# Performance work log

Hardware: AMD Instinct MI355X
Metric: run time of the kernel (lower is better)

The kernel has to match this reference:

```python
import math
import jax, jax.numpy as jnp
import numpy as np

T_NHEAD = 4
S_NHEAD = 4


def _ln(x, s, b, eps=1e-5):
    m = jnp.mean(x, axis=-1, keepdims=True)
    v = jnp.mean((x - m) ** 2, axis=-1, keepdims=True)
    return (x - m) / jnp.sqrt(v + eps) * s + b


def _pos_encoding(T, D):
    pos = jnp.arange(T, dtype=jnp.float32)[:, None]
    div = jnp.exp(jnp.arange(0, D, 2, dtype=jnp.float32) * (-math.log(10000.0) / D))
    pe = jnp.zeros((T, D), dtype=jnp.float32)
    pe = pe.at[:, 0::2].set(jnp.sin(pos * div))
    pe = pe.at[:, 1::2].set(jnp.cos(pos * div))
    return pe


def _forward(industry_ids, stock_features, market_features, emb_table, gate_w, gate_b,
             proj_w, proj_b, t_qw, t_kw, t_vw, t_ow, t_ob, t_nx_s, t_nx_b, t_nf_s, t_nf_b,
             t_f1w, t_f1b, t_f2w, t_f2b, s_qw, s_kw, s_vw, s_ow, s_ob, s_nx_s, s_nx_b,
             s_ni_s, s_ni_b, s_nf_s, s_nf_b, s_f1w, s_f1b, s_f2w, s_f2b, ta_w, dec_w, dec_b):
    N, T, F = stock_features.shape
    D = proj_w.shape[1]
    # industry embedding lookup
    ind_emb = emb_table[industry_ids]  # [N, E]
    # market gate (last timestep only), beta=1.0, scaled by d_output=d_feat
    mkt = market_features[:, -1, :]
    gate = F * jax.nn.softmax(mkt @ gate_w + gate_b, axis=-1)  # [N, F]
    x = stock_features * gate[:, None, :]
    # feature projection + positional encoding
    x = x @ proj_w + proj_b  # [N, T, D]
    x = x + _pos_encoding(T, D)
    # ---- TAttention (per-stock temporal self-attention) ----
    hd = D // T_NHEAD
    xs = _ln(x, t_nx_s, t_nx_b)
    q = (xs @ t_qw).reshape(N, T, T_NHEAD, hd)
    k = (xs @ t_kw).reshape(N, T, T_NHEAD, hd)
    v = (xs @ t_vw).reshape(N, T, T_NHEAD, hd)
    scores = jnp.einsum('nthd,nshd->nhts', q, k) / math.sqrt(hd)
    attn = jax.nn.softmax(scores, axis=-1)
    o = jnp.einsum('nhts,nshd->nthd', attn, v).reshape(N, T, D)
    xt = x + (o @ t_ow + t_ob)
    y = _ln(xt, t_nf_s, t_nf_b)
    xt = xt + (jax.nn.relu(y @ t_f1w + t_f1b) @ t_f2w + t_f2b)
    # ---- TemporalAttention (aggregate over time) ----
    h = xt @ ta_w  # [N, T, D]
    lam = jax.nn.softmax(jnp.einsum('ntd,nd->nt', h, h[:, -1, :]), axis=1)
    z = jnp.einsum('nt,ntd->nd', lam, xt)  # [N, D]
    # ---- SAttention (cross-stock attention over N) ----
    shd = D // S_NHEAD
    zs = _ln(z, s_nx_s, s_nx_b)
    ins = _ln(ind_emb, s_ni_s, s_ni_b)
    qk_in = jnp.concatenate([zs, ins], axis=-1)  # [N, D+E]
    sq = (qk_in @ s_qw).reshape(N, S_NHEAD, shd)
    sk = (qk_in @ s_kw).reshape(N, S_NHEAD, shd)
    sv = (zs @ s_vw).reshape(N, S_NHEAD, shd)
    sc = jnp.einsum('nhd,mhd->hnm', sq, sk) / math.sqrt(shd)
    sa = jax.nn.softmax(sc, axis=-1)
    so = jnp.einsum('hnm,mhd->nhd', sa, sv).reshape(N, D)
    zt = z + (so @ s_ow + s_ob)
    yn = _ln(zt, s_nf_s, s_nf_b)
    zt = zt + (jax.nn.relu(yn @ s_f1w + s_f1b) @ s_f2w + s_f2b)
    # decoder
    return zt @ dec_w + dec_b  # [N, 1]


def setup_inputs() -> dict:
    key = jax.random.key(0)
    ks = iter(jax.random.split(key, 64))
    N, T, F, M, E, D = 4096, 64, 158, 64, 32, 256
    def rn(shape, s=0.05):
        return jax.random.normal(next(ks), shape, dtype=jnp.float32) * s
    return dict(
        industry_ids=jax.random.randint(next(ks), (N,), 0, 256, dtype=jnp.int32),
        stock_features=rn((N, T, F), 1.0),
        market_features=rn((N, T, M), 1.0),
        emb_table=rn((256, E)),
        gate_w=rn((M, F)), gate_b=jnp.zeros((F,), jnp.float32),
        proj_w=rn((F, D)), proj_b=jnp.zeros((D,), jnp.float32),
        t_qw=rn((D, D)), t_kw=rn((D, D)), t_vw=rn((D, D)),
        t_ow=rn((D, D)), t_ob=jnp.zeros((D,), jnp.float32),
        t_nx_s=jnp.ones((D,), jnp.float32), t_nx_b=jnp.zeros((D,), jnp.float32),
        t_nf_s=jnp.ones((D,), jnp.float32), t_nf_b=jnp.zeros((D,), jnp.float32),
        t_f1w=rn((D, D)), t_f1b=jnp.zeros((D,), jnp.float32),
        t_f2w=rn((D, D)), t_f2b=jnp.zeros((D,), jnp.float32),
        s_qw=rn((D + E, D)), s_kw=rn((D + E, D)), s_vw=rn((D, D)),
        s_ow=rn((D, D)), s_ob=jnp.zeros((D,), jnp.float32),
        s_nx_s=jnp.ones((D,), jnp.float32), s_nx_b=jnp.zeros((D,), jnp.float32),
        s_ni_s=jnp.ones((E,), jnp.float32), s_ni_b=jnp.zeros((E,), jnp.float32),
        s_nf_s=jnp.ones((D,), jnp.float32), s_nf_b=jnp.zeros((D,), jnp.float32),
        s_f1w=rn((D, D)), s_f1b=jnp.zeros((D,), jnp.float32),
        s_f2w=rn((D, D)), s_f2b=jnp.zeros((D,), jnp.float32),
        ta_w=rn((D, D)),
        dec_w=rn((D, 1)), dec_b=jnp.zeros((1,), jnp.float32),
    )


def reference(industry_ids, stock_features, market_features, emb_table, gate_w, gate_b,
              proj_w, proj_b, t_qw, t_kw, t_vw, t_ow, t_ob, t_nx_s, t_nx_b, t_nf_s, t_nf_b,
              t_f1w, t_f1b, t_f2w, t_f2b, s_qw, s_kw, s_vw, s_ow, s_ob, s_nx_s, s_nx_b,
              s_ni_s, s_ni_b, s_nf_s, s_nf_b, s_f1w, s_f1b, s_f2w, s_f2b, ta_w, dec_w, dec_b):
    return _forward(industry_ids, stock_features, market_features, emb_table, gate_w, gate_b,
                    proj_w, proj_b, t_qw, t_kw, t_vw, t_ow, t_ob, t_nx_s, t_nx_b, t_nf_s, t_nf_b,
                    t_f1w, t_f1b, t_f2w, t_f2b, s_qw, s_kw, s_vw, s_ow, s_ob, s_nx_s, s_nx_b,
                    s_ni_s, s_ni_b, s_nf_s, s_nf_b, s_f1w, s_f1b, s_f2w, s_f2b, ta_w, dec_w, dec_b)
```

## Files before the change

kernel.cpp:

```cpp
#include <hip/hip_runtime.h>

typedef _Float16 f16;
typedef _Float16 f16x8 __attribute__((ext_vector_type(8)));
typedef _Float16 f16x4 __attribute__((ext_vector_type(4)));
typedef float    f32x4 __attribute__((ext_vector_type(4)));

#define MFMA32(a,b,c) __builtin_amdgcn_mfma_f32_16x16x32_f16((a),(b),(c),0,0,0)
#define MFMA16(a,b,c) __builtin_amdgcn_mfma_f32_16x16x16f16((a),(b),(c),0,0,0)

__device__ __forceinline__ f32x4 zero4() { f32x4 v = {0.f,0.f,0.f,0.f}; return v; }
#define ZERO44(A) { _Pragma("unroll") for (int z1=0;z1<4;++z1){ _Pragma("unroll") for (int z2=0;z2<4;++z2) A[z1][z2] = zero4(); } }

constexpr size_t OFF_PROJ = 0;
constexpr size_t OFF_QW  = 40960;
constexpr size_t OFF_KW  = 106496;
constexpr size_t OFF_VW  = 172032;
constexpr size_t OFF_OW  = 237568;
constexpr size_t OFF_F1  = 303104;
constexpr size_t OFF_F2  = 368640;
constexpr size_t OFF_TA  = 434176;
constexpr size_t OFF_SQW = 499712;
constexpr size_t OFF_SKW = 573440;
constexpr size_t OFF_SVW = 647168;
constexpr size_t OFF_SOW = 712704;
constexpr size_t OFF_SF1 = 778240;
constexpr size_t OFF_SF2 = 843776;
constexpr size_t W_ELEMS = 909312;
constexpr size_t PE_B  = W_ELEMS*2;
constexpr size_t Z_B   = PE_B  + 64*256*4;
constexpr size_t QK_B  = Z_B   + 4096ull*256*4;
constexpr size_t SQ_B  = QK_B  + 4096ull*288*2;
constexpr size_t SK_B  = SQ_B  + 4096ull*256*2;
constexpr size_t SVT_B = SK_B  + 4096ull*256*2;
constexpr size_t SO_B  = SVT_B + 4096ull*256*2;

struct PrepArgs {
  const float* src[14];
  int K[14]; int Kp[14]; int off[14];
};

__global__ void prep_kernel(PrepArgs a, f16* __restrict__ wbuf, float* __restrict__ pe) {
  int wsel = blockIdx.y;
  int tid = threadIdx.x;
  if (wsel < 14) {
    const float* S = a.src[wsel];
    int K = a.K[wsel], Kp = a.Kp[wsel];
    f16* D = wbuf + a.off[wsel];
    int n = blockIdx.x*4 + (tid & 3);
    for (int k = (tid >> 2); k < Kp; k += 64) {
      float v = (k < K) ? S[(size_t)k*256 + n] : 0.f;
      D[(size_t)n*Kp + k] = (f16)v;
    }
  } else {
    int idx = blockIdx.x*256 + tid;
    int t = idx >> 8, d = idx & 255, i = d >> 1;
    float div = expf((float)(2*i) * (-9.210340371976184f/256.f));
    float ang = (float)t * div;
    pe[idx] = (d & 1) ? cosf(ang) : sinf(ang);
  }
}

__device__ __forceinline__ void ln64v(f16 (*src)[264], f16 (*dst)[264],
    const float* __restrict__ sc, const float* __restrict__ bi, int w, int lane) {
  int row = w*16 + (lane >> 2);
  int c0 = lane & 3;
  f16x8 v[8];
  float s = 0.f, s2 = 0.f;
  #pragma unroll
  for (int j = 0; j < 8; ++j) {
    v[j] = *(const f16x8*)&src[row][j*32 + c0*8];
    #pragma unroll
    for (int e = 0; e < 8; ++e) { float f = (float)v[j][e]; s += f; s2 += f*f; }
  }
  s  += __shfl_xor(s, 1);  s  += __shfl_xor(s, 2);
  s2 += __shfl_xor(s2, 1); s2 += __shfl_xor(s2, 2);
  float mean = s * (1.f/256.f);
  float rstd = rsqrtf(s2 * (1.f/256.f) - mean*mean + 1e-5f);
  #pragma unroll
  for (int j = 0; j < 8; ++j) {
    int c = j*32 + c0*8;
    f16x8 o;
    #pragma unroll
    for (int e = 0; e < 8; ++e)
      o[e] = (f16)(((float)v[j][e] - mean) * rstd * sc[c+e] + bi[c+e]);
    *(f16x8*)&dst[row][c] = o;
  }
}

template<int KSTEPS, int LDB>
__device__ __forceinline__ void gemm_ldsA(f16 (*A)[264], const f16* __restrict__ B,
                                          f32x4 (&acc)[4][4], int w, int l15, int g) {
  #pragma unroll 2
  for (int ks = 0; ks < KSTEPS; ++ks) {
    int kc = ks*32 + g*8;
    f16x8 av[4], bv[4];
    #pragma unroll
    for (int j = 0; j < 4; ++j) av[j] = *(const f16x8*)&A[j*16 + l15][kc];
    #pragma unroll
    for (int j = 0; j < 4; ++j) bv[j] = *(const f16x8*)(B + (size_t)(w*64 + j*16 + l15)*LDB + kc);
    #pragma unroll
    for (int mt = 0; mt < 4; ++mt) {
      #pragma unroll
      for (int nt = 0; nt < 4; ++nt)
        acc[mt][nt] = MFMA32(av[mt], bv[nt], acc[mt][nt]);
    }
  }
}

__device__ __forceinline__ void ffn_block(f16 (*res)[264], f16 (*y)[264], f16 (*u)[72],
    const f16* __restrict__ W1, const f16* __restrict__ W2,
    const float* __restrict__ b1, const float* __restrict__ b2,
    int w, int l15, int g) {
  f32x4 acc2[4][4]; ZERO44(acc2);
  for (int ch = 0; ch < 4; ++ch) {
    f32x4 ua[4];
    #pragma unroll
    for (int nt = 0; nt < 4; ++nt) ua[nt] = zero4();
    #pragma unroll 2
    for (int ks = 0; ks < 8; ++ks) {
      int kc = ks*32 + g*8;
      f16x8 av = *(const f16x8*)&y[w*16 + l15][kc];
      f16x8 bv[4];
      #pragma unroll
      for (int j = 0; j < 4; ++j) bv[j] = *(const f16x8*)(W1 + (size_t)(ch*64 + j*16 + l15)*256 + kc);
      #pragma unroll
      for (int nt = 0; nt < 4; ++nt) ua[nt] = MFMA32(av, bv[nt], ua[nt]);
    }
    __syncthreads();
    #pragma unroll
    for (int nt = 0; nt < 4; ++nt) {
      int col = nt*16 + l15;
      #pragma unroll
      for (int i = 0; i < 4; ++i) {
        float v = ua[nt][i] + b1[ch*64 + col];
        u[w*16 + g*4 + i][col] = (f16)fmaxf(v, 0.f);
      }
    }
    __syncthreads();
    #pragma unroll
    for (int ks = 0; ks < 2; ++ks) {
      int kc = ks*32 + g*8;
      f16x8 av[4], bv[4];
      #pragma unroll
      for (int j = 0; j < 4; ++j) av[j] = *(const f16x8*)&u[j*16 + l15][kc];
      #pragma unroll
      for (int j = 0; j < 4; ++j) bv[j] = *(const f16x8*)(W2 + (size_t)(w*64 + j*16 + l15)*256 + ch*64 + kc);
      #pragma unroll
      for (int mt = 0; mt < 4; ++mt) {
        #pragma unroll
        for (int nt = 0; nt < 4; ++nt)
          acc2[mt][nt] = MFMA32(av[mt], bv[nt], acc2[mt][nt]);
      }
    }
  }
  #pragma unroll
  for (int mt = 0; mt < 4; ++mt) {
    #pragma unroll
    for (int nt = 0; nt < 4; ++nt) {
      int col = w*64 + nt*16 + l15;
      #pragma unroll
      for (int i = 0; i < 4; ++i) {
        int row = mt*16 + g*4 + i;
        float v = (float)res[row][col] + acc2[mt][nt][i] + b2[col];
        res[row][col] = (f16)v;
      }
    }
  }
}

__global__ __launch_bounds__(256, 2) void temporal_kernel(
    const float* __restrict__ stock, const float* __restrict__ market,
    const float* __restrict__ gate_w, const float* __restrict__ gate_b,
    const float* __restrict__ proj_b, const float* __restrict__ t_ob,
    const float* __restrict__ t_nx_s, const float* __restrict__ t_nx_b,
    const float* __restrict__ t_nf_s, const float* __restrict__ t_nf_b,
    const float* __restrict__ t_f1b, const float* __restrict__ t_f2b,
    const f16* __restrict__ wbuf, const float* __restrict__ pe,
    float* __restrict__ zout)
{
  __shared__ __align__(16) f16 B[64][264];
  __shared__ __align__(16) f16 ub[64][40];
  __shared__ float gatev[160];
  __shared__ float mkt[64];
  __shared__ float red[66];

  const int tid = threadIdx.x;
  const int lane = tid & 63;
  const int w = tid >> 6;
  const int l15 = lane & 15;
  const int g = lane >> 4;
  const int n = blockIdx.x;

  f16x4 xres[4][4];

  if (tid < 64) mkt[tid] = market[(size_t)n*4096 + 63*64 + tid];
  __syncthreads();
  float logit = 0.f;
  if (tid < 158) {
    float acc = gate_b[tid];
    for (int m = 0; m < 64; ++m) acc += mkt[m] * gate_w[m*158 + tid];
    logit = acc;
  }
  if (tid < 160) gatev[tid] = (tid < 158) ? logit : -1e30f;
  __syncthreads();
  if (w == 0) {
    float v = fmaxf(gatev[lane], gatev[lane + 64]);
    if (lane < 32) v = fmaxf(v, gatev[lane + 128]);
    #pragma unroll
    for (int off = 32; off >= 1; off >>= 1) v = fmaxf(v, __shfl_xor(v, off));
    if (lane == 0) red[0] = v;
  }
  __syncthreads();
  float gmax = red[0];
  float ev = (tid < 158) ? __expf(logit - gmax) : 0.f;
  if (tid < 160) gatev[tid] = ev;
  __syncthreads();
  if (w == 0) {
    float v = gatev[lane] + gatev[lane + 64] + ((lane < 32) ? gatev[lane + 128] : 0.f);
    #pragma unroll
    for (int off = 32; off >= 1; off >>= 1) v += __shfl_xor(v, off);
    if (lane == 0) red[1] = v;
  }
  __syncthreads();
  const float grs = 158.f / red[1];

  for (int idx = tid; idx < 64*158; idx += 256) {
    int t = idx / 158, f = idx - t*158;
    B[t][f] = (f16)(stock[(size_t)n*(64*158) + idx] * (gatev[f] * grs));
  }
  if (tid < 128) B[tid >> 1][158 + (tid & 1)] = (f16)0.f;
  __syncthreads();

  {
    f32x4 acc[4][4]; ZERO44(acc);
    gemm_ldsA<5,160>(B, wbuf + OFF_PROJ, acc, w, l15, g);
    __syncthreads();
    #pragma unroll
    for (int mt = 0; mt < 4; ++mt) {
      #pragma unroll
      for (int nt = 0; nt < 4; ++nt) {
        int col = w*64 + nt*16 + l15;
        #pragma unroll
        for (int i = 0; i < 4; ++i) {
          int row = mt*16 + g*4 + i;
          float vv = acc[mt][nt][i] + proj_b[col] + pe[row*256 + col];
          xres[mt][nt][i] = (f16)vv;
          B[row][col] = (f16)vv;
        }
      }
    }
  }
  __syncthreads();
  ln64v(B, B, t_nx_s, t_nx_b, w, lane);
  __syncthreads();

  {
    const int h = w;
    f32x4 sacc[4][4]; ZERO44(sacc);
    #pragma unroll
    for (int kd = 0; kd < 4; ++kd) {
      f32x4 qacc[4], kacc[4];
      #pragma unroll
      for (int nt = 0; nt < 4; ++nt) { qacc[nt] = zero4(); kacc[nt] = zero4(); }
      #pragma unroll 2
      for (int ks = 0; ks < 8; ++ks) {
        int kc = ks*32 + g*8;
        f16x8 xv[4];
        #pragma unroll
        for (int j = 0; j < 4; ++j) xv[j] = *(const f16x8*)&B[j*16 + l15][kc];
        f16x8 wq = *(const f16x8*)(wbuf + OFF_QW + (size_t)(h*64 + kd*16 + l15)*256 + kc);
        f16x8 wk = *(const f16x8*)(wbuf + OFF_KW + (size_t)(h*64 + kd*16 + l15)*256 + kc);
        #pragma unroll
        for (int nt = 0; nt < 4; ++nt) {
          qacc[nt] = MFMA32(wq, xv[nt], qacc[nt]);
          kacc[nt] = MFMA32(wk, xv[nt], kacc[nt]);
        }
      }
      f16x4 qf[4], kf[4];
      #pragma unroll
      for (int nt = 0; nt < 4; ++nt) {
        #pragma unroll
        for (int i = 0; i < 4; ++i) {
          qf[nt][i] = (f16)(qacc[nt][i] * 0.125f);
          kf[nt][i] = (f16)kacc[nt][i];
        }
      }
      #pragma unroll
      for (int ms = 0; ms < 4; ++ms) {
        #pragma unroll
        for (int nt = 0; nt < 4; ++nt)
          sacc[ms][nt] = MFMA16(kf[ms], qf[nt], sacc[ms][nt]);
      }
    }
    f16x4 pf[4][4];
    #pragma unroll
    for (int nt = 0; nt < 4; ++nt) {
      float mx = -1e30f;
      #pragma unroll
      for (int ms = 0; ms < 4; ++ms) {
        #pragma unroll
        for (int i = 0; i < 4; ++i) mx = fmaxf(mx, sacc[ms][nt][i]);
      }
      mx = fmaxf(mx, __shfl_xor(mx, 16));
      mx = fmaxf(mx, __shfl_xor(mx, 32));
      float sm = 0.f;
      #pragma unroll
      for (int ms = 0; ms < 4; ++ms) {
        #pragma unroll
        for (int i = 0; i < 4; ++i) { float e = __expf(sacc[ms][nt][i] - mx); sacc[ms][nt][i] = e; sm += e; }
      }
      sm += __shfl_xor(sm, 16);
      sm += __shfl_xor(sm, 32);
      float r = 1.f / sm;
      #pragma unroll
      for (int ms = 0; ms < 4; ++ms) {
        #pragma unroll
        for (int i = 0; i < 4; ++i) pf[ms][nt][i] = (f16)(sacc[ms][nt][i] * r);
      }
    }
    f32x4 oacc[4][4]; ZERO44(oacc);
    #pragma unroll
    for (int ks = 0; ks < 4; ++ks) {
      f32x4 vacc[4];
      #pragma unroll
      for (int nd = 0; nd < 4; ++nd) vacc[nd] = zero4();
      #pragma unroll 2
      for (int kk = 0; kk < 8; ++kk) {
        int kc = kk*32 + g*8;
        f16x8 xv = *(const f16x8*)&B[ks*16 + l15][kc];
        #pragma unroll
        for (int nd = 0; nd < 4; ++nd) {
          f16x8 wv = *(const f16x8*)(wbuf + OFF_VW + (size_t)(h*64 + nd*16 + l15)*256 + kc);
          vacc[nd] = MFMA32(xv, wv, vacc[nd]);
        }
      }
      f16x4 vf[4];
      #pragma unroll
      for (int nd = 0; nd < 4; ++nd) {
        #pragma unroll
        for (int i = 0; i < 4; ++i) vf[nd][i] = (f16)vacc[nd][i];
      }
      #pragma unroll
      for (int md = 0; md < 4; ++md) {
        #pragma unroll
        for (int nt = 0; nt < 4; ++nt)
          oacc[md][nt] = MFMA16(vf[md], pf[ks][nt], oacc[md][nt]);
      }
    }
    __syncthreads();
    #pragma unroll
    for (int md = 0; md < 4; ++md) {
      #pragma unroll
      for (int nt = 0; nt < 4; ++nt) {
        int t = nt*16 + l15;
        f16x4 ov;
        #pragma unroll
        for (int i = 0; i < 4; ++i) ov[i] = (f16)oacc[md][nt][i];
        *(f16x4*)&B[t][h*64 + md*16 + g*4] = ov;
      }
    }
  }
  __syncthreads();

  {
    f32x4 acc[4][4]; ZERO44(acc);
    gemm_ldsA<8,256>(B, wbuf + OFF_OW, acc, w, l15, g);
    __syncthreads();
    #pragma unroll
    for (int mt = 0; mt < 4; ++mt) {
      #pragma unroll
      for (int nt = 0; nt < 4; ++nt) {
        int col = w*64 + nt*16 + l15;
        #pragma unroll
        for (int i = 0; i < 4; ++i) {
          int row = mt*16 + g*4 + i;
          float vv = (float)xres[mt][nt][i] + acc[mt][nt][i] + t_ob[col];
          xres[mt][nt][i] = (f16)vv;
          B[row][col] = (f16)vv;
        }
      }
    }
  }
  __syncthreads();
  ln64v(B, B, t_nf_s, t_nf_b, w, lane);
  __syncthreads();

  {
    f32x4 acc2[4][4]; ZERO44(acc2);
    for (int ch = 0; ch < 8; ++ch) {
      f32x4 ua[2];
      ua[0] = zero4(); ua[1] = zero4();
      #pragma unroll 2
      for (int ks = 0; ks < 8; ++ks) {
        int kc = ks*32 + g*8;
        f16x8 av = *(const f16x8*)&B[w*16 + l15][kc];
        f16x8 bv0 = *(const f16x8*)(wbuf + OFF_F1 + (size_t)(ch*32 + l15)*256 + kc);
        f16x8 bv1 = *(const f16x8*)(wbuf + OFF_F1 + (size_t)(ch*32 + 16 + l15)*256 + kc);
        ua[0] = MFMA32(av, bv0, ua[0]);
        ua[1] = MFMA32(av, bv1, ua[1]);
      }
      __syncthreads();
      #pragma unroll
      for (int nt = 0; nt < 2; ++nt) {
        int col = nt*16 + l15;
        #pragma unroll
        for (int i = 0; i < 4; ++i) {
          float v = ua[nt][i] + t_f1b[ch*32 + col];
          ub[w*16 + g*4 + i][col] = (f16)fmaxf(v, 0.f);
        }
      }
      __syncthreads();
      {
        int kc = g*8;
        f16x8 av[4], bv[4];
        #pragma unroll
        for (int j = 0; j < 4; ++j) av[j] = *(const f16x8*)&ub[j*16 + l15][kc];
        #pragma unroll
        for (int j = 0; j < 4; ++j) bv[j] = *(const f16x8*)(wbuf + OFF_F2 + (size_t)(w*64 + j*16 + l15)*256 + ch*32 + kc);
        #pragma unroll
        for (int mt = 0; mt < 4; ++mt) {
          #pragma unroll
          for (int nt = 0; nt < 4; ++nt)
            acc2[mt][nt] = MFMA32(av[mt], bv[nt], acc2[mt][nt]);
        }
      }
    }
    #pragma unroll
    for (int mt = 0; mt < 4; ++mt) {
      #pragma unroll
      for (int nt = 0; nt < 4; ++nt) {
        int col = w*64 + nt*16 + l15;
        #pragma unroll
        for (int i = 0; i < 4; ++i) {
          int row = mt*16 + g*4 + i;
          float vv = (float)xres[mt][nt][i] + acc2[mt][nt][i] + t_f2b[col];
          xres[mt][nt][i] = (f16)vv;
          B[row][col] = (f16)vv;
        }
      }
    }
  }
  __syncthreads();

  {
    f32x4 acc[4][4]; ZERO44(acc);
    gemm_ldsA<8,256>(B, wbuf + OFF_TA, acc, w, l15, g);
    __syncthreads();
    #pragma unroll
    for (int mt = 0; mt < 4; ++mt) {
      #pragma unroll
      for (int nt = 0; nt < 4; ++nt) {
        int col = w*64 + nt*16 + l15;
        #pragma unroll
        for (int i = 0; i < 4; ++i) B[mt*16 + g*4 + i][col] = (f16)acc[mt][nt][i];
      }
    }
  }
  __syncthreads();

  {
    int row = w*16 + (lane >> 2);
    int c0 = lane & 3;
    float dt = 0.f;
    #pragma unroll
    for (int j = 0; j < 8; ++j) {
      f16x8 va = *(const f16x8*)&B[row][j*32 + c0*8];
      f16x8 vb = *(const f16x8*)&B[63][j*32 + c0*8];
      #pragma unroll
      for (int e = 0; e < 8; ++e) dt += (float)va[e] * (float)vb[e];
    }
    dt += __shfl_xor(dt, 1); dt += __shfl_xor(dt, 2);
    if (c0 == 0) red[2 + row] = dt;
  }
  __syncthreads();
  if (tid < 64) {
    float v = red[2 + tid];
    float mx = v;
    #pragma unroll
    for (int off = 32; off >= 1; off >>= 1) mx = fmaxf(mx, __shfl_xor(mx, off));
    float e = __expf(v - mx);
    float sm = e;
    #pragma unroll
    for (int off = 32; off >= 1; off >>= 1) sm += __shfl_xor(sm, off);
    red[2 + tid] = e / sm;
  }
  __syncthreads();
  {
    float zacc[4] = {0.f, 0.f, 0.f, 0.f};
    #pragma unroll
    for (int mt = 0; mt < 4; ++mt) {
      #pragma unroll
      for (int i = 0; i < 4; ++i) {
        float l = red[2 + mt*16 + g*4 + i];
        #pragma unroll
        for (int nt = 0; nt < 4; ++nt) zacc[nt] += l * (float)xres[mt][nt][i];
      }
    }
    #pragma unroll
    for (int nt = 0; nt < 4; ++nt) {
      zacc[nt] += __shfl_xor(zacc[nt], 16);
      zacc[nt] += __shfl_xor(zacc[nt], 32);
    }
    if (g == 0) {
      #pragma unroll
      for (int nt = 0; nt < 4; ++nt)
        zout[(size_t)n*256 + w*64 + nt*16 + l15] = zacc[nt];
    }
  }
}

__global__ __launch_bounds__(256) void qkin_kernel(
    const float* __restrict__ z, const int* __restrict__ ids,
    const float* __restrict__ emb,
    const float* __restrict__ s_nx_s, const float* __restrict__ s_nx_b,
    const float* __restrict__ s_ni_s, const float* __restrict__ s_ni_b,
    f16* __restrict__ qk)
{
  int lane = threadIdx.x & 63;
  int w = threadIdx.x >> 6;
  int r = blockIdx.x*4 + w;
  const float* zr = z + (size_t)r*256;
  float v[4]; float s = 0.f, s2 = 0.f;
  #pragma unroll
  for (int j = 0; j < 4; ++j) { v[j] = zr[lane*4 + j]; s += v[j]; s2 += v[j]*v[j]; }
  #pragma unroll
  for (int off = 32; off >= 1; off >>= 1) { s += __shfl_xor(s, off); s2 += __shfl_xor(s2, off); }
  float mean = s*(1.f/256.f);
  float rstd = rsqrtf(s2*(1.f/256.f) - mean*mean + 1e-5f);
  f16* q = qk + (size_t)r*288;
  #pragma unroll
  for (int j = 0; j < 4; ++j) {
    int c = lane*4 + j;
    q[c] = (f16)((v[j] - mean)*rstd*s_nx_s[c] + s_nx_b[c]);
  }
  int id = ids[r];
  float e = (lane < 32) ? emb[id*32 + lane] : 0.f;
  float es = e, es2 = e*e;
  #pragma unroll
  for (int off = 16; off >= 1; off >>= 1) { es += __shfl_xor(es, off); es2 += __shfl_xor(es2, off); }
  if (lane < 32) {
    float m2 = es*(1.f/32.f);
    float rs2 = rsqrtf(es2*(1.f/32.f) - m2*m2 + 1e-5f);
    q[256 + lane] = (f16)((e - m2)*rs2*s_ni_s[lane] + s_ni_b[lane]);
  }
}

__global__ __launch_bounds__(256) void sqk_kernel(const f16* __restrict__ qk,
    const f16* __restrict__ wbuf, f16* __restrict__ sq, f16* __restrict__ sk)
{
  const int tid = threadIdx.x, lane = tid & 63, w = tid >> 6, l15 = lane & 15, g = lane >> 4;
  const int isk = blockIdx.y;
  const f16* W = wbuf + (isk ? OFF_SKW : OFF_SQW);
  f16* out = isk ? sk : sq;
  const float scale = isk ? 1.f : 0.125f;
  const int r0 = blockIdx.x*64;
  f32x4 acc[4][4]; ZERO44(acc);
  #pragma unroll 2
  for (int ks = 0; ks < 9; ++ks) {
    int kc = ks*32 + g*8;
    f16x8 av[4], bv[4];
    #pragma unroll
    for (int j = 0; j < 4; ++j) av[j] = *(const f16x8*)(qk + (size_t)(r0 + j*16 + l15)*288 + kc);
    #pragma unroll
    for (int j = 0; j < 4; ++j) bv[j] = *(const f16x8*)(W + (size_t)(w*64 + j*16 + l15)*288 + kc);
    #pragma unroll
    for (int mt = 0; mt < 4; ++mt) {
      #pragma unroll
      for (int nt = 0; nt < 4; ++nt) acc[mt][nt] = MFMA32(av[mt], bv[nt], acc[mt][nt]);
    }
  }
  #pragma unroll
  for (int mt = 0; mt < 4; ++mt) {
    #pragma unroll
    for (int nt = 0; nt < 4; ++nt) {
      int col = w*64 + nt*16 + l15;
      #pragma unroll
      for (int i = 0; i < 4; ++i)
        out[(size_t)(r0 + mt*16 + g*4 + i)*256 + col] = (f16)(acc[mt][nt][i]*scale);
    }
  }
}

__global__ __launch_bounds__(256) void svt_kernel(const f16* __restrict__ qk,
    const f16* __restrict__ wbuf, f16* __restrict__ svT)
{
  const int tid = threadIdx.x, lane = tid & 63, w = tid >> 6, l15 = lane & 15, g = lane >> 4;
  const int k0 = blockIdx.x*64;
  f32x4 acc[4][4]; ZERO44(acc);
  #pragma unroll 2
  for (int ks = 0; ks < 8; ++ks) {
    int kc = ks*32 + g*8;
    f16x8 av[4], bv[4];
    #pragma unroll
    for (int j = 0; j < 4; ++j) av[j] = *(const f16x8*)(wbuf + OFF_SVW + (size_t)(w*64 + j*16 + l15)*256 + kc);
    #pragma unroll
    for (int j = 0; j < 4; ++j) bv[j] = *(const f16x8*)(qk + (size_t)(k0 + j*16 + l15)*288 + kc);
    #pragma unroll
    for (int md = 0; md < 4; ++md) {
      #pragma unroll
      for (int nk = 0; nk < 4; ++nk) acc[md][nk] = MFMA32(av[md], bv[nk], acc[md][nk]);
    }
  }
  #pragma unroll
  for (int md = 0; md < 4; ++md) {
    #pragma unroll
    for (int nk = 0; nk < 4; ++nk) {
      int key = k0 + nk*16 + l15;
      #pragma unroll
      for (int i = 0; i < 4; ++i)
        svT[(size_t)(w*64 + md*16 + g*4 + i)*4096 + key] = (f16)acc[md][nk][i];
    }
  }
}

__global__ __launch_bounds__(256) void xattn_kernel(const f16* __restrict__ sq,
    const f16* __restrict__ sk, const f16* __restrict__ svT, f16* __restrict__ so)
{
  const int lane = threadIdx.x & 63, w = threadIdx.x >> 6, l15 = lane & 15, g = lane >> 4;
  const int h = blockIdx.y;
  const int q0 = blockIdx.x*64 + w*16;
  const f16* qp = sq + (size_t)q0*256 + h*64;
  f16x8 qf0 = *(const f16x8*)(qp + (size_t)l15*256 + g*8);
  f16x8 qf1 = *(const f16x8*)(qp + (size_t)l15*256 + 32 + g*8);
  f32x4 oacc[4];
  #pragma unroll
  for (int md = 0; md < 4; ++md) oacc[md] = zero4();
  float mrun = -1e30f, lrun = 0.f;
  for (int kt = 0; kt < 64; ++kt) {
    const f16* kp = sk + (size_t)kt*64*256 + h*64;
    f32x4 sacc[4];
    #pragma unroll
    for (int mt = 0; mt < 4; ++mt) sacc[mt] = zero4();
    #pragma unroll
    for (int mt = 0; mt < 4; ++mt) {
      f16x8 k0f = *(const f16x8*)(kp + (size_t)(mt*16 + l15)*256 + g*8);
      f16x8 k1f = *(const f16x8*)(kp + (size_t)(mt*16 + l15)*256 + 32 + g*8);
      sacc[mt] = MFMA32(k0f, qf0, sacc[mt]);
      sacc[mt] = MFMA32(k1f, qf1, sacc[mt]);
    }
    float tmax = -1e30f;
    #pragma unroll
    for (int mt = 0; mt < 4; ++mt) {
      #pragma unroll
      for (int i = 0; i < 4; ++i) tmax = fmaxf(tmax, sacc[mt][i]);
    }
    tmax = fmaxf(tmax, __shfl_xor(tmax, 16));
    tmax = fmaxf(tmax, __shfl_xor(tmax, 32));
    float mnew = fmaxf(mrun, tmax);
    float corr = __expf(mrun - mnew);
    float ts = 0.f;
    #pragma unroll
    for (int mt = 0; mt < 4; ++mt) {
      #pragma unroll
      for (int i = 0; i < 4; ++i) { float e = __expf(sacc[mt][i] - mnew); sacc[mt][i] = e; ts += e; }
    }
    ts += __shfl_xor(ts, 16);
    ts += __shfl_xor(ts, 32);
    lrun = lrun*corr + ts;
    mrun = mnew;
    f16x4 pf[4];
    #pragma unroll
    for (int mt = 0; mt < 4; ++mt) {
      #pragma unroll
      for (int i = 0; i < 4; ++i) pf[mt][i] = (f16)sacc[mt][i];
    }
    #pragma unroll
    for (int md = 0; md < 4; ++md) {
      #pragma unroll
      for (int i = 0; i < 4; ++i) oacc[md][i] *= corr;
    }
    const f16* vp = svT + (size_t)h*64*4096 + kt*64;
    #pragma unroll
    for (int ks = 0; ks < 4; ++ks) {
      #pragma unroll
      for (int md = 0; md < 4; ++md) {
        f16x4 vf = *(const f16x4*)(vp + (size_t)(md*16 + l15)*4096 + ks*16 + g*4);
        oacc[md] = MFMA16(vf, pf[ks], oacc[md]);
      }
    }
  }
  float rinv = 1.f / lrun;
  #pragma unroll
  for (int md = 0; md < 4; ++md) {
    f16x4 ov;
    #pragma unroll
    for (int i = 0; i < 4; ++i) ov[i] = (f16)(oacc[md][i]*rinv);
    *(f16x4*)(so + (size_t)(q0 + l15)*256 + h*64 + md*16 + g*4) = ov;
  }
}

__global__ __launch_bounds__(256, 2) void final_kernel(
    const f16* __restrict__ so, const float* __restrict__ z,
    const f16* __restrict__ wbuf,
    const float* __restrict__ s_ob,
    const float* __restrict__ s_nf_s, const float* __restrict__ s_nf_b,
    const float* __restrict__ s_f1b, const float* __restrict__ s_f2b,
    const float* __restrict__ dec_w, const float* __restrict__ dec_b,
    float* __restrict__ out)
{
  __shared__ __align__(16) f16 zb[64][264];
  __shared__ __align__(16) f16 yb[64][264];
  __shared__ __align__(16) f16 ub[64][72];
  const int tid = threadIdx.x, lane = tid & 63, w = tid >> 6, l15 = lane & 15, g = lane >> 4;
  const int r0 = blockIdx.x*64;
  {
    f32x4 acc[4][4]; ZERO44(acc);
    #pragma unroll 2
    for (int ks = 0; ks < 8; ++ks) {
      int kc = ks*32 + g*8;
      f16x8 av[4], bv[4];
      #pragma unroll
      for (int j = 0; j < 4; ++j) av[j] = *(const f16x8*)(so + (size_t)(r0 + j*16 + l15)*256 + kc);
      #pragma unroll
      for (int j = 0; j < 4; ++j) bv[j] = *(const f16x8*)(wbuf + OFF_SOW + (size_t)(w*64 + j*16 + l15)*256 + kc);
      #pragma unroll
      for (int mt = 0; mt < 4; ++mt) {
        #pragma unroll
        for (int nt = 0; nt < 4; ++nt) acc[mt][nt] = MFMA32(av[mt], bv[nt], acc[mt][nt]);
      }
    }
    #pragma unroll
    for (int mt = 0; mt < 4; ++mt) {
      #pragma unroll
      for (int nt = 0; nt < 4; ++nt) {
        int col = w*64 + nt*16 + l15;
        #pragma unroll
        for (int i = 0; i < 4; ++i) {
          int row = mt*16 + g*4 + i;
          zb[row][col] = (f16)(z[(size_t)(r0 + row)*256 + col] + acc[mt][nt][i] + s_ob[col]);
        }
      }
    }
  }
  __syncthreads();
  ln64v(zb, yb, s_nf_s, s_nf_b, w, lane);
  __syncthreads();
  ffn_block(zb, yb, ub, wbuf + OFF_SF1, wbuf + OFF_SF2, s_f1b, s_f2b, w, l15, g);
  __syncthreads();
  {
    int row = w*16 + (lane >> 2), c0 = lane & 3;
    float dt = 0.f;
    #pragma unroll
    for (int j = 0; j < 8; ++j) {
      f16x8 va = *(const f16x8*)&zb[row][j*32 + c0*8];
      #pragma unroll
      for (int e = 0; e < 8; ++e) dt += (float)va[e]*dec_w[j*32 + c0*8 + e];
    }
    dt += __shfl_xor(dt, 1); dt += __shfl_xor(dt, 2);
    if (c0 == 0) out[r0 + row] = dt + dec_b[0];
  }
}

extern "C" void kernel_launch(void* const* d_in, const int* in_sizes, int n_in,
                              void* d_out, int out_size, void* d_ws, size_t ws_size,
                              hipStream_t stream)
{
  const int*   ids    = (const int*)  d_in[0];
  const float* stock  = (const float*)d_in[1];
  const float* market = (const float*)d_in[2];
  const float* emb    = (const float*)d_in[3];
  const float* gate_w = (const float*)d_in[4];
  const float* gate_b = (const float*)d_in[5];

  char* ws = (char*)d_ws;
  f16*   wbuf = (f16*)ws;
  float* pe   = (float*)(ws + PE_B);
  float* zbuf = (float*)(ws + Z_B);
  f16*   qk   = (f16*)(ws + QK_B);
  f16*   sq   = (f16*)(ws + SQ_B);
  f16*   sk   = (f16*)(ws + SK_B);
  f16*   svT  = (f16*)(ws + SVT_B);
  f16*   so   = (f16*)(ws + SO_B);

  PrepArgs pa;
  const int srcIdx[14] = {6,8,9,10,11,17,19,36,21,22,23,24,32,34};
  const int Ks[14]   = {158,256,256,256,256,256,256,256,288,288,256,256,256,256};
  const int Kps[14]  = {160,256,256,256,256,256,256,256,288,288,256,256,256,256};
  const int offs[14] = {(int)OFF_PROJ,(int)OFF_QW,(int)OFF_KW,(int)OFF_VW,(int)OFF_OW,
                        (int)OFF_F1,(int)OFF_F2,(int)OFF_TA,(int)OFF_SQW,(int)OFF_SKW,
                        (int)OFF_SVW,(int)OFF_SOW,(int)OFF_SF1,(int)OFF_SF2};
  for (int i = 0; i < 14; ++i) {
    pa.src[i] = (const float*)d_in[srcIdx[i]];
    pa.K[i] = Ks[i]; pa.Kp[i] = Kps[i]; pa.off[i] = offs[i];
  }

  prep_kernel<<<dim3(64,15), dim3(256), 0, stream>>>(pa, wbuf, pe);
  temporal_kernel<<<dim3(4096), dim3(256), 0, stream>>>(
      stock, market, gate_w, gate_b,
      (const float*)d_in[7],  (const float*)d_in[12],
      (const float*)d_in[13], (const float*)d_in[14],
      (const float*)d_in[15], (const float*)d_in[16],
      (const float*)d_in[18], (const float*)d_in[20],
      wbuf, pe, zbuf);
  qkin_kernel<<<dim3(1024), dim3(256), 0, stream>>>(
      zbuf, ids, emb,
      (const float*)d_in[26], (const float*)d_in[27],
      (const float*)d_in[28], (const float*)d_in[29], qk);
  sqk_kernel<<<dim3(64,2), dim3(256), 0, stream>>>(qk, wbuf, sq, sk);
  svt_kernel<<<dim3(64), dim3(256), 0, stream>>>(qk, wbuf, svT);
  xattn_kernel<<<dim3(64,4), dim3(256), 0, stream>>>(sq, sk, svT, so);
  final_kernel<<<dim3(64), dim3(256), 0, stream>>>(
      so, zbuf, wbuf,
      (const float*)d_in[25], (const float*)d_in[30], (const float*)d_in[31],
      (const float*)d_in[33], (const float*)d_in[35],
      (const float*)d_in[37], (const float*)d_in[38], (float*)d_out);
}
```

Before: 1.101 ms.

## Split temporal attention into query halves to cut registers and raise occupancy

The per-head attention is restructured into two passes, each covering half of the query tiles, and some inner loops now unroll by 1 instead of 2. Launch bounds go from 2 to 3 blocks per CU. The goal is lower peak VGPR pressure so more waves fit per CU. In exchange, the K and V projections are recomputed in each half, roughly doubling that MFMA work and its weight loads, and there is less unrolling for latency hiding.

```diff
diff --git a/kernel.cpp b/kernel.cpp
--- a/kernel.cpp
+++ b/kernel.cpp
@@ -90,7 +90,7 @@
 template<int KSTEPS, int LDB>
 __device__ __forceinline__ void gemm_ldsA(f16 (*A)[264], const f16* __restrict__ B,
                                           f32x4 (&acc)[4][4], int w, int l15, int g) {
-  #pragma unroll 2
+  #pragma unroll 1
   for (int ks = 0; ks < KSTEPS; ++ks) {
     int kc = ks*32 + g*8;
     f16x8 av[4], bv[4];
@@ -103,6 +103,128 @@
       #pragma unroll
       for (int nt = 0; nt < 4; ++nt)
         acc[mt][nt] = MFMA32(av[mt], bv[nt], acc[mt][nt]);
+    }
+  }
+}
+
+template<int TH2>
+__device__ __forceinline__ void attn_half(f16 (*B)[264], const f16* __restrict__ wbuf,
+                                          int h, int l15, int g, f16x4 (&of)[4][2]) {
+  f32x4 sacc[4][2];
+  #pragma unroll
+  for (int ms = 0; ms < 4; ++ms) { sacc[ms][0] = zero4(); sacc[ms][1] = zero4(); }
+  #pragma unroll
+  for (int kd = 0; kd < 4; ++kd) {
+    f16x4 kf[4];
+    {
+      f32x4 kacc[4];
+      #pragma unroll
+      for (int j = 0; j < 4; ++j) kacc[j] = zero4();
+      #pragma unroll 1
+      for (int ks = 0; ks < 8; ++ks) {
+        int kc = ks*32 + g*8;
+        f16x8 wk = *(const f16x8*)(wbuf + OFF_KW + (size_t)(h*64 + kd*16 + l15)*256 + kc);
+        #pragma unroll
+        for (int ms = 0; ms < 4; ++ms) {
+          f16x8 xv = *(const f16x8*)&B[ms*16 + l15][kc];
+          kacc[ms] = MFMA32(wk, xv, kacc[ms]);
+        }
+      }
+      #pragma unroll
+      for (int ms = 0; ms < 4; ++ms) {
+        #pragma unroll
+        for (int i = 0; i < 4; ++i) kf[ms][i] = (f16)kacc[ms][i];
+      }
+    }
+    f16x4 qf[2];
+    {
+      f32x4 qacc[2];
+      qacc[0] = zero4(); qacc[1] = zero4();
+      #pragma unroll 1
+      for (int ks = 0; ks < 8; ++ks) {
+        int kc = ks*32 + g*8;
+        f16x8 wq = *(const f16x8*)(wbuf + OFF_QW + (size_t)(h*64 + kd*16 + l15)*256 + kc);
+        f16x8 xv0 = *(const f16x8*)&B[(TH2*2 + 0)*16 + l15][kc];
+        f16x8 xv1 = *(const f16x8*)&B[(TH2*2 + 1)*16 + l15][kc];
+        qacc[0] = MFMA32(wq, xv0, qacc[0]);
+        qacc[1] = MFMA32(wq, xv1, qacc[1]);
+      }
+      #pragma unroll
+      for (int nt = 0; nt < 2; ++nt) {
+        #pragma unroll
+        for (int i = 0; i < 4; ++i) qf[nt][i] = (f16)(qacc[nt][i] * 0.125f);
+      }
+    }
+    #pragma unroll
+    for (int ms = 0; ms < 4; ++ms) {
+      #pragma unroll
+      for (int nt = 0; nt < 2; ++nt)
+        sacc[ms][nt] = MFMA16(kf[ms], qf[nt], sacc[ms][nt]);
+    }
+  }
+  f16x4 pf[4][2];
+  #pragma unroll
+  for (int nt = 0; nt < 2; ++nt) {
+    float mx = -1e30f;
+    #pragma unroll
+    for (int ms = 0; ms < 4; ++ms) {
+      #pragma unroll
+      for (int i = 0; i < 4; ++i) mx = fmaxf(mx, sacc[ms][nt][i]);
+    }
+    mx = fmaxf(mx, __shfl_xor(mx, 16));
+    mx = fmaxf(mx, __shfl_xor(mx, 32));
+    float sm = 0.f;
+    #pragma unroll
+    for (int ms = 0; ms < 4; ++ms) {
+      #pragma unroll
+      for (int i = 0; i < 4; ++i) { float e = __expf(sacc[ms][nt][i] - mx); sacc[ms][nt][i] = e; sm += e; }
+    }
+    sm += __shfl_xor(sm, 16);
+    sm += __shfl_xor(sm, 32);
+    float r = 1.f / sm;
+    #pragma unroll
+    for (int ms = 0; ms < 4; ++ms) {
+      #pragma unroll
+      for (int i = 0; i < 4; ++i) pf[ms][nt][i] = (f16)(sacc[ms][nt][i] * r);
+    }
+  }
+  f32x4 oacc[4][2];
+  #pragma unroll
+  for (int md = 0; md < 4; ++md) { oacc[md][0] = zero4(); oacc[md][1] = zero4(); }
+  #pragma unroll
+  for (int ks = 0; ks < 4; ++ks) {
+    f32x4 vacc[4];
+    #pragma unroll
+    for (int nd = 0; nd < 4; ++nd) vacc[nd] = zero4();
+    #pragma unroll 1
+    for (int kk = 0; kk < 8; ++kk) {
+      int kc = kk*32 + g*8;
+      f16x8 xv = *(const f16x8*)&B[ks*16 + l15][kc];
+      #pragma unroll
+      for (int nd = 0; nd < 4; ++nd) {
+        f16x8 wv = *(const f16x8*)(wbuf + OFF_VW + (size_t)(h*64 + nd*16 + l15)*256 + kc);
+        vacc[nd] = MFMA32(xv, wv, vacc[nd]);
+      }
+    }
+    f16x4 vf[4];
+    #pragma unroll
+    for (int nd = 0; nd < 4; ++nd) {
+      #pragma unroll
+      for (int i = 0; i < 4; ++i) vf[nd][i] = (f16)vacc[nd][i];
+    }
+    #pragma unroll
+    for (int md = 0; md < 4; ++md) {
+      #pragma unroll
+      for (int nt = 0; nt < 2; ++nt)
+        oacc[md][nt] = MFMA16(vf[md], pf[ks][nt], oacc[md][nt]);
+    }
+  }
+  #pragma unroll
+  for (int md = 0; md < 4; ++md) {
+    #pragma unroll
+    for (int nt = 0; nt < 2; ++nt) {
+      #pragma unroll
+      for (int i = 0; i < 4; ++i) of[md][nt][i] = (f16)oacc[md][nt][i];
     }
   }
 }
@@ -168,7 +290,7 @@
   }
 }
 
-__global__ __launch_bounds__(256, 2) void temporal_kernel(
+__global__ __launch_bounds__(256, 3) void temporal_kernel(
     const float* __restrict__ stock, const float* __restrict__ market,
     const float* __restrict__ gate_w, const float* __restrict__ gate_b,
     const float* __restrict__ proj_b, const float* __restrict__ t_ob,
@@ -256,107 +378,16 @@
 
   {
     const int h = w;
-    f32x4 sacc[4][4]; ZERO44(sacc);
-    #pragma unroll
-    for (int kd = 0; kd < 4; ++kd) {
-      f32x4 qacc[4], kacc[4];
-      #pragma unroll
-      for (int nt = 0; nt < 4; ++nt) { qacc[nt] = zero4(); kacc[nt] = zero4(); }
-      #pragma unroll 2
-      for (int ks = 0; ks < 8; ++ks) {
-        int kc = ks*32 + g*8;
-        f16x8 xv[4];
-        #pragma unroll
-        for (int j = 0; j < 4; ++j) xv[j] = *(const f16x8*)&B[j*16 + l15][kc];
-        f16x8 wq = *(const f16x8*)(wbuf + OFF_QW + (size_t)(h*64 + kd*16 + l15)*256 + kc);
-        f16x8 wk = *(const f16x8*)(wbuf + OFF_KW + (size_t)(h*64 + kd*16 + l15)*256 + kc);
-        #pragma unroll
-        for (int nt = 0; nt < 4; ++nt) {
-          qacc[nt] = MFMA32(wq, xv[nt], qacc[nt]);
-          kacc[nt] = MFMA32(wk, xv[nt], kacc[nt]);
-        }
-      }
-      f16x4 qf[4], kf[4];
-      #pragma unroll
-      for (int nt = 0; nt < 4; ++nt) {
-        #pragma unroll
-        for (int i = 0; i < 4; ++i) {
-          qf[nt][i] = (f16)(qacc[nt][i] * 0.125f);
-          kf[nt][i] = (f16)kacc[nt][i];
-        }
-      }
-      #pragma unroll
-      for (int ms = 0; ms < 4; ++ms) {
-        #pragma unroll
-        for (int nt = 0; nt < 4; ++nt)
-          sacc[ms][nt] = MFMA16(kf[ms], qf[nt], sacc[ms][nt]);
-      }
-    }
-    f16x4 pf[4][4];
-    #pragma unroll
-    for (int nt = 0; nt < 4; ++nt) {
-      float mx = -1e30f;
-      #pragma unroll
-      for (int ms = 0; ms < 4; ++ms) {
-        #pragma unroll
-        for (int i = 0; i < 4; ++i) mx = fmaxf(mx, sacc[ms][nt][i]);
-      }
-      mx = fmaxf(mx, __shfl_xor(mx, 16));
-      mx = fmaxf(mx, __shfl_xor(mx, 32));
-      float sm = 0.f;
-      #pragma unroll
-      for (int ms = 0; ms < 4; ++ms) {
-        #pragma unroll
-        for (int i = 0; i < 4; ++i) { float e = __expf(sacc[ms][nt][i] - mx); sacc[ms][nt][i] = e; sm += e; }
-      }
-      sm += __shfl_xor(sm, 16);
-      sm += __shfl_xor(sm, 32);
-      float r = 1.f / sm;
-      #pragma unroll
-      for (int ms = 0; ms < 4; ++ms) {
-        #pragma unroll
-        for (int i = 0; i < 4; ++i) pf[ms][nt][i] = (f16)(sacc[ms][nt][i] * r);
-      }
-    }
-    f32x4 oacc[4][4]; ZERO44(oacc);
-    #pragma unroll
-    for (int ks = 0; ks < 4; ++ks) {
-      f32x4 vacc[4];
-      #pragma unroll
-      for (int nd = 0; nd < 4; ++nd) vacc[nd] = zero4();
-      #pragma unroll 2
-      for (int kk = 0; kk < 8; ++kk) {
-        int kc = kk*32 + g*8;
-        f16x8 xv = *(const f16x8*)&B[ks*16 + l15][kc];
-        #pragma unroll
-        for (int nd = 0; nd < 4; ++nd) {
-          f16x8 wv = *(const f16x8*)(wbuf + OFF_VW + (size_t)(h*64 + nd*16 + l15)*256 + kc);
-          vacc[nd] = MFMA32(xv, wv, vacc[nd]);
-        }
-      }
-      f16x4 vf[4];
-      #pragma unroll
-      for (int nd = 0; nd < 4; ++nd) {
-        #pragma unroll
-        for (int i = 0; i < 4; ++i) vf[nd][i] = (f16)vacc[nd][i];
-      }
-      #pragma unroll
-      for (int md = 0; md < 4; ++md) {
-        #pragma unroll
-        for (int nt = 0; nt < 4; ++nt)
-          oacc[md][nt] = MFMA16(vf[md], pf[ks][nt], oacc[md][nt]);
-      }
-    }
+    f16x4 of0[4][2], of1[4][2];
+    attn_half<0>(B, wbuf, h, l15, g, of0);
+    attn_half<1>(B, wbuf, h, l15, g, of1);
     __syncthreads();
     #pragma unroll
     for (int md = 0; md < 4; ++md) {
       #pragma unroll
-      for (int nt = 0; nt < 4; ++nt) {
-        int t = nt*16 + l15;
-        f16x4 ov;
-        #pragma unroll
-        for (int i = 0; i < 4; ++i) ov[i] = (f16)oacc[md][nt][i];
-        *(f16x4*)&B[t][h*64 + md*16 + g*4] = ov;
+      for (int nt = 0; nt < 2; ++nt) {
+        *(f16x4*)&B[nt*16 + l15][h*64 + md*16 + g*4]       = of0[md][nt];
+        *(f16x4*)&B[(2 + nt)*16 + l15][h*64 + md*16 + g*4] = of1[md][nt];
       }
     }
   }
@@ -390,7 +421,7 @@
     for (int ch = 0; ch < 8; ++ch) {
       f32x4 ua[2];
       ua[0] = zero4(); ua[1] = zero4();
-      #pragma unroll 2
+      #pragma unroll 1
       for (int ks = 0; ks < 8; ++ks) {
         int kc = ks*32 + g*8;
         f16x8 av = *(const f16x8*)&B[w*16 + l15][kc];
```

Result: slower. 1.550 ms (+40.8%).
